# Optimization experiments

Measured on AMD Instinct MI355X. Metric: run time of the kernel, lower is better.

## Reference

```python
import jax, jax.numpy as jnp
import numpy as np
import math

B, T, M, C, H = 2, 2048, 1024, 512, 8
D = C // H  # head dim = 64


def setup_inputs() -> dict:
    key = jax.random.key(0)
    ks = jax.random.split(key, 6)
    return {
        "x": jax.random.normal(ks[0], (B, T, C), jnp.float32),
        "y": jax.random.normal(ks[1], (B, M, C), jnp.float32),
        "attn_x_mask": jnp.ones((1, 1, T, T), jnp.int32),
        "qkv_w": jax.random.normal(ks[2], (3 * C, C), jnp.float32) * 0.02,
        "qkv_b": jax.random.normal(ks[3], (3 * C,), jnp.float32) * 0.02,
        "proj_w": jax.random.normal(ks[4], (C, C), jnp.float32) * 0.02,
        "proj_b": jax.random.normal(ks[5], (C,), jnp.float32) * 0.02,
    }


def _split_heads(t, n, d):
    # [B, N, C] -> [B, H, N, D]
    b = t.shape[0]
    return t.reshape(b, n, H, d).transpose(0, 2, 1, 3)


def reference(x, y, attn_x_mask, qkv_w, qkv_b, proj_w, proj_b):
    b, t, c = x.shape
    m = y.shape[1]
    d = c // H
    scale = 1.0 / math.sqrt(d)

    # shared qkv projection applied to x and y (torch Linear: x @ W.T + b)
    qkv_x = x @ qkv_w.T + qkv_b
    q_x, k_x, v_x = jnp.split(qkv_x, 3, axis=-1)
    qkv_y = y @ qkv_w.T + qkv_b
    q_y, k_y, v_y = jnp.split(qkv_y, 3, axis=-1)

    q_x, k_x, v_x = (_split_heads(a, t, d) for a in (q_x, k_x, v_x))
    q_y, k_y, v_y = (_split_heads(a, m, d) for a in (q_y, k_y, v_y))

    # x -> y cross attention scores (pre-softmax, reused for chaining)
    catt_x2y = jnp.einsum("bhtd,bhmd->bhtm", q_x, k_y) * scale  # [B,H,T,M]
    cval_x2y = jnp.einsum("bhtm,bhmd->bhtd", jax.nn.softmax(catt_x2y, axis=-1), v_y)
    cval_x2y = cval_x2y.transpose(0, 2, 1, 3).reshape(b, t, c)

    # y -> x scores, then chained through raw x2y scores
    catt_y2x = jnp.einsum("bhmd,bhsd->bhms", q_y, k_x) * scale  # [B,H,M,T]
    chained = jnp.einsum("bhtm,bhms->bhts", catt_x2y, catt_y2x) * scale  # [B,H,T,T]
    chained = jnp.where(attn_x_mask == 0, -jnp.inf, chained)
    cval_y2x = jnp.einsum("bhts,bhsd->bhtd", jax.nn.softmax(chained, axis=-1), v_x)
    cval_y2x = cval_y2x.transpose(0, 2, 1, 3).reshape(b, t, c)

    out = cval_x2y - cval_y2x
    out = out @ proj_w.T + proj_b  # dropout layers are identity in eval mode
    return out
```

## Files before the change

### kernel.cpp

```cpp
#include <hip/hip_runtime.h>


typedef _Float16 half_t;
typedef _Float16 half8 __attribute__((ext_vector_type(8)));
typedef _Float16 half4v __attribute__((ext_vector_type(4)));
typedef float floatx4 __attribute__((ext_vector_type(4)));
typedef int int4v __attribute__((ext_vector_type(4)));
typedef int int2v __attribute__((ext_vector_type(2)));

constexpr int Bc = 2, Tc = 2048, Mc = 1024, Cc = 512, Hc = 8, Dc = 64;
constexpr long BTC = (long)Bc * Tc * Cc;
constexpr long ZT  = (long)Bc * Hc * Tc;
constexpr float S1 = 0.18033688f;

enum { EPI_F16STORE = 0, EPI_QKV_XY = 1, EPI_PROJ = 2 };

struct EpiParams {
  half_t* h0;
  half_t* h1;
  half_t* h2;
  half_t* h3;
  half_t* h4;
  half_t* h5;
  half_t* h6;
  float* f0;
  const float* bias;
  float scale;
  int ldc;
  long bstride;
};

__device__ __forceinline__ void gld_lds16(const half_t* g, half_t* l) {
  __builtin_amdgcn_global_load_lds(
      (const __attribute__((address_space(1))) void*)g,
      (__attribute__((address_space(3))) void*)l, 16, 0, 0);
}

__device__ __forceinline__ int pkrtz(float a, float b) {
  return __builtin_bit_cast(int, __builtin_amdgcn_cvt_pkrtz(a, b));
}
__device__ __forceinline__ void pl16(int& a, int& b) {
  asm volatile("v_permlane16_swap_b32 %0, %1" : "+v"(a), "+v"(b));
}
__device__ __forceinline__ void pl32(int& a, int& b) {
  asm volatile("v_permlane32_swap_b32 %0, %1" : "+v"(a), "+v"(b));
}

template <int BM, int BN, int WMG, int WNG, int EPI, int GX = 0, int GY = 0>
__global__ __launch_bounds__(256) void gemm_nt(
    const half_t* __restrict__ A, const half_t* __restrict__ Bt,
    int K, int lda, int ldb, long bsA, long bsB, EpiParams ep)
{
  constexpr int BK = 64;
  constexpr int WTM = BM / WMG, WTN = BN / WNG;
  constexpr int MI = WTM / 16, NI = WTN / 16;
  constexpr int AIT = BM * BK / 8 / 256;
  constexpr int BIT = BN * BK / 8 / 256;
  constexpr int NLD = AIT + BIT;
  __shared__ __align__(16) half_t As[2][BM * BK];
  __shared__ __align__(16) half_t Bs[2][BN * BK];

  const int tid = threadIdx.x;
  const int lane = tid & 63;
  const int wave = tid >> 6;
  const int wm = wave / WNG, wn = wave % WNG;
  const int r16 = lane & 15, g = lane >> 4;
  const int z = blockIdx.z;

  int bxl = blockIdx.x, byl = blockIdx.y;
  if constexpr (GX > 0) {
    constexpr int CHUNK = GX * GY / 8;
    const int f = byl * GX + bxl;
    const int L = (f & 7) * CHUNK + (f >> 3);
    bxl = L % GX; byl = L / GX;
  }
  const long m0 = (long)byl * BM;
  const long n0 = (long)bxl * BN;
  const half_t* Abase = A + (long)z * bsA + m0 * (long)lda;
  const half_t* Bbase = Bt + (long)z * bsB + n0 * (long)ldb;

  const int rA = wm * WTM + r16;
  const int rB = wn * WTN + r16;

  floatx4 acc[MI][NI];
#pragma unroll
  for (int mi = 0; mi < MI; ++mi)
#pragma unroll
    for (int ni = 0; ni < NI; ++ni)
      acc[mi][ni] = floatx4{0.f, 0.f, 0.f, 0.f};

  auto stage = [&](int kt, int buf) {
#pragma unroll
    for (int i = 0; i < AIT; ++i) {
      const int c = tid + i * 256;
      const int row = c >> 3, js = c & 7;
      const int jg = js ^ (row & 7);
      gld_lds16(Abase + (long)row * lda + kt + jg * 8, &As[buf][c * 8]);
    }
#pragma unroll
    for (int i = 0; i < BIT; ++i) {
      const int c = tid + i * 256;
      const int row = c >> 3, js = c & 7;
      const int jg = js ^ (row & 7);
      gld_lds16(Bbase + (long)row * ldb + kt + jg * 8, &Bs[buf][c * 8]);
    }
  };

  const int NIT = K / BK;
  stage(0, 0);
  asm volatile("" ::: "memory");

  for (int it = 0; it < NIT; ++it) {
    const bool hn = (it + 1 < NIT);
    if (hn) stage((it + 1) * BK, (it + 1) & 1);
    asm volatile("" ::: "memory");
    if (hn) {
      if constexpr (NLD == 6) asm volatile("s_waitcnt vmcnt(6)" ::: "memory");
      else if constexpr (NLD == 4) asm volatile("s_waitcnt vmcnt(4)" ::: "memory");
      else if constexpr (NLD == 3) asm volatile("s_waitcnt vmcnt(3)" ::: "memory");
      else if constexpr (NLD == 8) asm volatile("s_waitcnt vmcnt(8)" ::: "memory");
      else asm volatile("s_waitcnt vmcnt(0)" ::: "memory");
    } else {
      asm volatile("s_waitcnt vmcnt(0)" ::: "memory");
    }
    __builtin_amdgcn_s_barrier();
    asm volatile("" ::: "memory");

    const half_t* Ab = As[it & 1];
    const half_t* Bb = Bs[it & 1];
    half8 aF[MI][2], bF[NI][2];
#pragma unroll
    for (int mi = 0; mi < MI; ++mi)
#pragma unroll
      for (int k2 = 0; k2 < 2; ++k2)
        aF[mi][k2] = *reinterpret_cast<const half8*>(
            &Ab[(rA + mi * 16) * BK + ((k2 * 4 + g) ^ (r16 & 7)) * 8]);
#pragma unroll
    for (int ni = 0; ni < NI; ++ni)
#pragma unroll
      for (int k2 = 0; k2 < 2; ++k2)
        bF[ni][k2] = *reinterpret_cast<const half8*>(
            &Bb[(rB + ni * 16) * BK + ((k2 * 4 + g) ^ (r16 & 7)) * 8]);
    __builtin_amdgcn_s_setprio(1);
#pragma unroll
    for (int k2 = 0; k2 < 2; ++k2)
#pragma unroll
      for (int mi = 0; mi < MI; ++mi)
#pragma unroll
        for (int ni = 0; ni < NI; ++ni)
          acc[mi][ni] = __builtin_amdgcn_mfma_f32_16x16x32_f16(
              aF[mi][k2], bF[ni][k2], acc[mi][ni], 0, 0, 0);
    __builtin_amdgcn_s_setprio(0);
    asm volatile("s_waitcnt lgkmcnt(0)" ::: "memory");
    __builtin_amdgcn_s_barrier();
    asm volatile("" ::: "memory");
  }

  half_t* Txp = &As[0][0];
  const bool isx  = (m0 < (long)Bc * Tc);
  const int which = (int)(n0 >> 9);
  const int hh    = ((int)n0 & 511) >> 6;

#pragma unroll
  for (int mi = 0; mi < MI; ++mi) {
#pragma unroll
    for (int ni = 0; ni < NI; ++ni) {
#pragma unroll
      for (int reg = 0; reg < 4; ++reg) {
        const int r = (int)m0 + wm * WTM + mi * 16 + g * 4 + reg;
        const int c = (int)n0 + wn * WTN + ni * 16 + r16;
        const float v = acc[mi][ni][reg];
        if constexpr (EPI == EPI_F16STORE) {
          ep.h0[(long)z * ep.bstride + (long)r * ep.ldc + c] = (half_t)(v * ep.scale);
        } else if constexpr (EPI == EPI_QKV_XY) {
          const float val = v + ep.bias[c];
          const int d = c & 63;
          const int rloc = r - (int)m0;
          if (isx) {
            const int b = (int)(m0 >> 11);
            const int t = r & (Tc - 1);
            const long bh = (long)(b * Hc + hh);
            if (which == 0)      ep.h0[(bh * Tc + t) * Dc + d] = (half_t)(val * S1);
            else if (which == 1) ep.h1[(bh * Tc + t) * Dc + d] = (half_t)val;
            else                 Txp[d * 136 + rloc] = (half_t)val;
          } else {
            const long m2 = m0 - (long)Bc * Tc;
            const int b = (int)(m2 >> 10);
            const int t = (r - Bc * Tc) & (Mc - 1);
            const long bh = (long)(b * Hc + hh);
            if (which == 0)      Txp[d * 136 + rloc] = (half_t)(val * 0.125f);
            else if (which == 1) { ep.h4[(bh * Mc + t) * Dc + d] = (half_t)val;
                                   Txp[d * 136 + rloc] = (half_t)val; }
            else                 Txp[d * 136 + rloc] = (half_t)val;
          }
        } else {
          ep.f0[(long)r * Cc + c] = v + ep.bias[c];
        }
      }
    }
  }

  if constexpr (EPI == EPI_QKV_XY && BM == 128) {
    const bool hasT = isx ? (which == 2) : true;
    if (hasT) {
      __syncthreads();
      half_t* dstT; int L; long tb; int b;
      if (isx) { dstT = ep.h2; L = Tc; tb = m0 & (Tc - 1); b = (int)(m0 >> 11); }
      else {
        const long m2 = m0 - (long)Bc * Tc;
        b = (int)(m2 >> 10); tb = m2 & (Mc - 1); L = Mc;
        dstT = (which == 0) ? ep.h3 : (which == 1) ? ep.h5 : ep.h6;
      }
      const long bh = (long)(b * Hc + hh);
      const int dr = tid >> 2, qd = tid & 3;
      half_t* gbase = dstT + (bh * 64 + dr) * L + tb + qd * 32;
#pragma unroll
      for (int j = 0; j < 4; ++j) {
        const half8 v8 = *reinterpret_cast<const half8*>(&Txp[dr * 136 + qd * 32 + j * 8]);
        *reinterpret_cast<half8*>(&gbase[j * 8]) = v8;
      }
    }
  }
}

__global__ __launch_bounds__(256) void wtq2(
    const half_t* __restrict__ QYT, const half_t* __restrict__ KYT,
    const half_t* __restrict__ QX, half_t* __restrict__ Q2)
{
  __shared__ __align__(16) half_t As[2][4096];
  __shared__ __align__(16) half_t Bs[2][4096];
  __shared__ __align__(16) half_t WTs[4096];
  const int tid = threadIdx.x, lane = tid & 63, wave = tid >> 6;
  const int wm = wave >> 1, wn = wave & 1;
  const int r16 = lane & 15, g = lane >> 4;
  const int f = blockIdx.x;
  const int L = (f & 7) * 64 + (f >> 3);
  const int z = L >> 5;
  const int t0 = (L & 31) * 64;
  const half_t* Aq = QYT + (long)z * Dc * Mc;
  const half_t* Bk = KYT + (long)z * Dc * Mc;

  auto stage1 = [&](int kt, int buf) {
#pragma unroll
    for (int i = 0; i < 2; ++i) {
      const int c = tid + i * 256;
      const int row = c >> 3, js = c & 7, jg = js ^ (row & 7);
      gld_lds16(Aq + (long)row * Mc + kt + jg * 8, &As[buf][c * 8]);
    }
#pragma unroll
    for (int i = 0; i < 2; ++i) {
      const int c = tid + i * 256;
      const int row = c >> 3, js = c & 7, jg = js ^ (row & 7);
      gld_lds16(Bk + (long)row * Mc + kt + jg * 8, &Bs[buf][c * 8]);
    }
  };

  floatx4 acc[2][2];
#pragma unroll
  for (int mi = 0; mi < 2; ++mi)
#pragma unroll
    for (int ni = 0; ni < 2; ++ni) acc[mi][ni] = floatx4{0.f, 0.f, 0.f, 0.f};

  const int rA = wm * 32 + r16, rB = wn * 32 + r16;
  stage1(0, 0);
  asm volatile("" ::: "memory");
  for (int it = 0; it < 16; ++it) {
    const bool hn = (it < 15);
    if (hn) stage1((it + 1) * 64, (it + 1) & 1);
    asm volatile("" ::: "memory");
    if (hn) asm volatile("s_waitcnt vmcnt(4)" ::: "memory");
    else    asm volatile("s_waitcnt vmcnt(0)" ::: "memory");
    __builtin_amdgcn_s_barrier();
    asm volatile("" ::: "memory");
    const half_t* Ab = As[it & 1];
    const half_t* Bb = Bs[it & 1];
    half8 aF[2][2], bF[2][2];
#pragma unroll
    for (int mi = 0; mi < 2; ++mi)
#pragma unroll
      for (int k2 = 0; k2 < 2; ++k2)
        aF[mi][k2] = *reinterpret_cast<const half8*>(
            &Ab[(rA + mi * 16) * 64 + ((k2 * 4 + g) ^ (r16 & 7)) * 8]);
#pragma unroll
    for (int ni = 0; ni < 2; ++ni)
#pragma unroll
      for (int k2 = 0; k2 < 2; ++k2)
        bF[ni][k2] = *reinterpret_cast<const half8*>(
            &Bb[(rB + ni * 16) * 64 + ((k2 * 4 + g) ^ (r16 & 7)) * 8]);
    __builtin_amdgcn_s_setprio(1);
#pragma unroll
    for (int k2 = 0; k2 < 2; ++k2)
#pragma unroll
      for (int mi = 0; mi < 2; ++mi)
#pragma unroll
        for (int ni = 0; ni < 2; ++ni)
          acc[mi][ni] = __builtin_amdgcn_mfma_f32_16x16x32_f16(
              aF[mi][k2], bF[ni][k2], acc[mi][ni], 0, 0, 0);
    __builtin_amdgcn_s_setprio(0);
    asm volatile("s_waitcnt lgkmcnt(0)" ::: "memory");
    __builtin_amdgcn_s_barrier();
    asm volatile("" ::: "memory");
  }

  half_t* P2 = &As[0][0];
#pragma unroll
  for (int i = 0; i < 2; ++i) {
    const int c = tid + i * 256;
    const int row = c >> 3, js = c & 7, jg = js ^ (row & 7);
    gld_lds16(QX + ((long)z * Tc + t0 + row) * 64 + jg * 8, P2 + c * 8);
  }
#pragma unroll
  for (int mi = 0; mi < 2; ++mi)
#pragma unroll
    for (int ni = 0; ni < 2; ++ni)
#pragma unroll
      for (int reg = 0; reg < 4; ++reg) {
        const int r = wm * 32 + mi * 16 + g * 4 + reg;
        const int c = wn * 32 + ni * 16 + r16;
        WTs[r * 64 + (((c >> 3) ^ (r & 7)) << 3) + (c & 7)] =
            (half_t)(acc[mi][ni][reg] * 0.125f);
      }
  __syncthreads();

  floatx4 a2[4];
#pragma unroll
  for (int ni = 0; ni < 4; ++ni) a2[ni] = floatx4{0.f, 0.f, 0.f, 0.f};
  const int rA2 = wave * 16 + r16;
  half8 aF2[2], bF2[4][2];
#pragma unroll
  for (int k2 = 0; k2 < 2; ++k2)
    aF2[k2] = *reinterpret_cast<const half8*>(
        &P2[rA2 * 64 + ((k2 * 4 + g) ^ (r16 & 7)) * 8]);
#pragma unroll
  for (int ni = 0; ni < 4; ++ni)
#pragma unroll
    for (int k2 = 0; k2 < 2; ++k2)
      bF2[ni][k2] = *reinterpret_cast<const half8*>(
          &WTs[(ni * 16 + r16) * 64 + ((k2 * 4 + g) ^ (r16 & 7)) * 8]);
#pragma unroll
  for (int k2 = 0; k2 < 2; ++k2)
#pragma unroll
    for (int ni = 0; ni < 4; ++ni)
      a2[ni] = __builtin_amdgcn_mfma_f32_16x16x32_f16(
          aF2[k2], bF2[ni][k2], a2[ni], 0, 0, 0);
#pragma unroll
  for (int ni = 0; ni < 4; ++ni)
#pragma unroll
    for (int reg = 0; reg < 4; ++reg) {
      const int t = t0 + wave * 16 + g * 4 + reg;
      const int c = ni * 16 + r16;
      Q2[((long)z * Tc + t) * 64 + c] = (half_t)a2[ni][reg];
    }
}

__device__ __forceinline__ void stageK64(const half_t* Kz, int s0, half_t* dst, int tid) {
#pragma unroll
  for (int i = 0; i < 2; ++i) {
    const int c = tid + i * 256;
    const int row = c >> 3, js = c & 7;
    const int jg = js ^ (row & 7);
    gld_lds16(Kz + (long)(s0 + row) * 64 + jg * 8, dst + c * 8);
  }
}
__device__ __forceinline__ void stageV64(const half_t* Vz, int s0, int Slen, half_t* dst, int tid) {
#pragma unroll
  for (int i = 0; i < 2; ++i) {
    const int c = tid + i * 256;
    const int row = c >> 3, js = c & 7;
    const int jg = js ^ (row & 7);
    gld_lds16(Vz + (long)row * Slen + s0 + jg * 8, dst + c * 8);
  }
}

template <bool MASKED>
__device__ __forceinline__ void flash_body(
    const half_t* __restrict__ Qp, const half_t* __restrict__ Kp,
    const half_t* __restrict__ Vp, const unsigned char* __restrict__ mpk,
    half_t* __restrict__ POh, float* __restrict__ Lp,
    int Slen, int sbeg, int z, int q0, half_t* lds)
{
  const int tid = threadIdx.x, lane = tid & 63, w = tid >> 6;
  const int r16 = lane & 15, g = lane >> 4;
  const int b = z >> 3, h = z & 7;
  const int NT = Slen >> 7;
  const half_t* Qz = Qp + ((long)z * Tc + q0) * 64;
  const half_t* Kz = Kp + (long)z * Slen * 64;
  const half_t* Vz = Vp + (long)z * 64 * Slen;
  half_t* Kb0 = lds;
  half_t* Kb1 = lds + 4096;
  half_t* Vb  = lds + 8192;

  stageK64(Kz, sbeg, Kb0, tid);
  asm volatile("" ::: "memory");
  stageV64(Vz, sbeg, Slen, Vb, tid);
  asm volatile("" ::: "memory");

  half8 aQ[2][2];
#pragma unroll
  for (int mi = 0; mi < 2; ++mi)
#pragma unroll
    for (int k2 = 0; k2 < 2; ++k2)
      aQ[mi][k2] = *reinterpret_cast<const half8*>(
          Qz + (w * 32 + mi * 16 + r16) * 64 + k2 * 32 + g * 8);

  half8 vones;
#pragma unroll
  for (int j = 0; j < 8; ++j) vones[j] = (half_t)1.f;

  floatx4 oaccT[2][4];
  floatx4 lacc4[2];
#pragma unroll
  for (int mi = 0; mi < 2; ++mi) {
    lacc4[mi] = floatx4{0.f, 0.f, 0.f, 0.f};
#pragma unroll
    for (int no = 0; no < 4; ++no) oaccT[mi][no] = floatx4{0.f, 0.f, 0.f, 0.f};
  }

  const int send = sbeg + 512;
  int cur = 0;
  for (int s0 = sbeg; s0 < send; s0 += 64) {
    const bool hn = (s0 + 64 < send);
    asm volatile("s_waitcnt vmcnt(2)" ::: "memory");
    __builtin_amdgcn_s_barrier();
    asm volatile("" ::: "memory");

    unsigned int mb32[2];
    if constexpr (MASKED) {
      const int tile = s0 >> 7;
#pragma unroll
      for (int mi = 0; mi < 2; ++mi) {
        const int q = q0 + w * 32 + mi * 16 + r16;
        mb32[mi] = *reinterpret_cast<const unsigned int*>(
            mpk + ((long)q * NT + tile) * 16 + 4 * g);
      }
    }
    const int hf4 = ((s0 >> 6) & 1) ? 4 : 0;
    const unsigned int fullm = hf4 ? 0xf0f0f0f0u : 0x0f0f0f0fu;

    floatx4 sacc[2][4];
#pragma unroll
    for (int mi = 0; mi < 2; ++mi)
#pragma unroll
      for (int ni = 0; ni < 4; ++ni) sacc[mi][ni] = floatx4{0.f, 0.f, 0.f, 0.f};
    const half_t* Kc = cur ? Kb1 : Kb0;
    __builtin_amdgcn_s_setprio(1);
#pragma unroll
    for (int ni = 0; ni < 4; ++ni) {
      const int rB = ni * 16 + r16;
      const half8 b0 = *reinterpret_cast<const half8*>(&Kc[rB * 64 + (g ^ (rB & 7)) * 8]);
      const half8 b1 = *reinterpret_cast<const half8*>(&Kc[rB * 64 + ((4 + g) ^ (rB & 7)) * 8]);
#pragma unroll
      for (int mi = 0; mi < 2; ++mi) {
        sacc[mi][ni] = __builtin_amdgcn_mfma_f32_16x16x32_f16(b0, aQ[mi][0], sacc[mi][ni], 0, 0, 0);
        sacc[mi][ni] = __builtin_amdgcn_mfma_f32_16x16x32_f16(b1, aQ[mi][1], sacc[mi][ni], 0, 0, 0);
      }
    }
    __builtin_amdgcn_s_setprio(0);
    if (hn) stageK64(Kz, s0 + 64, cur ? Kb0 : Kb1, tid);
    asm volatile("" ::: "memory");

#pragma unroll
    for (int mi = 0; mi < 2; ++mi) {
      if constexpr (MASKED) {
        if ((mb32[mi] & fullm) != fullm) {
#pragma unroll
          for (int reg = 0; reg < 4; ++reg)
#pragma unroll
            for (int ni = 0; ni < 4; ++ni)
              if (!((mb32[mi] >> (reg * 8 + ni + hf4)) & 1)) sacc[mi][ni][reg] = -__builtin_inff();
        }
      }
#pragma unroll
      for (int ni = 0; ni < 4; ++ni)
#pragma unroll
        for (int reg = 0; reg < 4; ++reg)
          sacc[mi][ni][reg] = __builtin_amdgcn_exp2f(sacc[mi][ni][reg]);
    }

    if (hn) { asm volatile("s_waitcnt vmcnt(2)" ::: "memory"); }
    else    { asm volatile("s_waitcnt vmcnt(0)" ::: "memory"); }
    __builtin_amdgcn_s_barrier();
    asm volatile("" ::: "memory");

#pragma unroll
    for (int c = 0; c < 2; ++c) {
      half8 bVv[4];
#pragma unroll
      for (int no = 0; no < 4; ++no) {
        const int rV = no * 16 + r16;
        bVv[no] = *reinterpret_cast<const half8*>(
            &Vb[rV * 64 + ((c * 4 + g) ^ (rV & 7)) * 8]);
      }
#pragma unroll
      for (int mi = 0; mi < 2; ++mi) {
        int x0 = pkrtz(sacc[mi][2 * c][0],     sacc[mi][2 * c][1]);
        int x1 = pkrtz(sacc[mi][2 * c][2],     sacc[mi][2 * c][3]);
        int x2 = pkrtz(sacc[mi][2 * c + 1][0], sacc[mi][2 * c + 1][1]);
        int x3 = pkrtz(sacc[mi][2 * c + 1][2], sacc[mi][2 * c + 1][3]);
        pl32(x0, x2); pl32(x1, x3);
        pl16(x0, x2); pl16(x1, x3);
        int4v wv; wv[0] = x0; wv[1] = x1; wv[2] = x2; wv[3] = x3;
        const half8 aP = __builtin_bit_cast(half8, wv);
        __builtin_amdgcn_s_setprio(1);
#pragma unroll
        for (int no = 0; no < 4; ++no)
          oaccT[mi][no] = __builtin_amdgcn_mfma_f32_16x16x32_f16(bVv[no], aP, oaccT[mi][no], 0, 0, 0);
        lacc4[mi] = __builtin_amdgcn_mfma_f32_16x16x32_f16(vones, aP, lacc4[mi], 0, 0, 0);
        __builtin_amdgcn_s_setprio(0);
      }
    }
    __builtin_amdgcn_s_barrier();
    asm volatile("" ::: "memory");
    if (hn) stageV64(Vz, s0 + 64, Slen, Vb, tid);
    asm volatile("" ::: "memory");
    cur ^= 1;
  }

  float ls2[2];
#pragma unroll
  for (int mi = 0; mi < 2; ++mi) ls2[mi] = lacc4[mi][0];

  float* slab = reinterpret_cast<float*>(lds) + w * 1024;
#pragma unroll
  for (int mi = 0; mi < 2; ++mi) {
    const int tq = q0 + w * 32 + mi * 16;
    if (lane < 16) Lp[(long)z * Tc + tq + r16] = ls2[mi];
#pragma unroll
    for (int no = 0; no < 4; ++no) {
      floatx4 v = oaccT[mi][no];
      *reinterpret_cast<floatx4*>(&slab[r16 * 64 + no * 16 + (g ^ (r16 & 3)) * 4]) = v;
    }
#pragma unroll
    for (int it = 0; it < 4; ++it) {
      const int q2 = it * 4 + g;
      const int d4 = r16;
      const floatx4 v = *reinterpret_cast<const floatx4*>(
          &slab[q2 * 64 + (d4 >> 2) * 16 + ((d4 & 3) ^ (q2 & 3)) * 4]);
      const long off = ((long)(b * Tc + tq + q2)) * Cc + h * 64 + d4 * 4;
      half4v hh; hh[0] = (half_t)v[0]; hh[1] = (half_t)v[1];
      hh[2] = (half_t)v[2]; hh[3] = (half_t)v[3];
      __builtin_nontemporal_store(__builtin_bit_cast(int2v, hh),
                                  reinterpret_cast<int2v*>(&POh[off]));
    }
  }
}

__global__ __launch_bounds__(256, 4) void flash_both(
    const half_t* __restrict__ Q2, const half_t* __restrict__ KX,
    const half_t* __restrict__ VXT, const unsigned char* __restrict__ mpk,
    const half_t* __restrict__ QX, const half_t* __restrict__ KY,
    const half_t* __restrict__ VYT,
    half_t* __restrict__ POh, float* __restrict__ Lp)
{
  __shared__ __align__(16) half_t lds[12288];
  const int bx = blockIdx.x;
  if (bx < 1024) {
    const int z  = ((bx & 7) << 1) | ((bx >> 3) & 1);
    const int qt = (bx >> 4) & 3;
    const int q0 = (bx >> 6) * 128;
    flash_body<true>(Q2, KX, VXT, mpk,
                     POh + (long)qt * BTC, Lp + (long)qt * ZT,
                     Tc, qt * 512, z, q0, lds);
  } else {
    const int b2 = bx - 1024;
    const int z  = ((b2 & 7) << 1) | ((b2 >> 3) & 1);
    const int sh = (b2 >> 4) & 1;
    const int q0 = (b2 >> 5) * 128;
    flash_body<false>(QX, KY, VYT, nullptr,
                      POh + (long)(4 + sh) * BTC, Lp + (long)(4 + sh) * ZT,
                      Mc, sh * 512, z, q0, lds);
  }
}

__global__ __launch_bounds__(256) void combine_k(
    const half_t* __restrict__ POh, const float* __restrict__ Lp,
    half_t* __restrict__ DH)
{
  const long idx = (long)blockIdx.x * 256 + threadIdx.x;
  const long c8 = idx * 8;
  const int c = (int)(c8 & (Cc - 1));
  const long bt = c8 >> 9;
  const int h = c >> 6;
  const int b = (int)(bt >> 11), t = (int)(bt & (Tc - 1));
  const long zt = (long)(b * Hc + h) * Tc + t;
  const float i0 = 1.f / (Lp[zt] + Lp[ZT + zt] + Lp[2 * ZT + zt] + Lp[3 * ZT + zt]);
  const float i1 = 1.f / (Lp[4 * ZT + zt] + Lp[5 * ZT + zt]);
  half8 o[6];
#pragma unroll
  for (int s = 0; s < 6; ++s)
    o[s] = __builtin_bit_cast(half8, __builtin_nontemporal_load(
        reinterpret_cast<const int4v*>(POh) + s * (BTC / 8) + idx));
  half8 r;
#pragma unroll
  for (int j = 0; j < 8; ++j) {
    float a0 = 0.f, a1 = 0.f;
#pragma unroll
    for (int s = 0; s < 4; ++s) a0 += (float)o[s][j];
#pragma unroll
    for (int s = 4; s < 6; ++s) a1 += (float)o[s][j];
    r[j] = (half_t)(a1 * i1 - a0 * i0);
  }
  *reinterpret_cast<half8*>(&DH[c8]) = r;
}

__device__ __forceinline__ void cvt4(const float* in, half_t* out, long i) {
  const float4 f = reinterpret_cast<const float4*>(in)[i];
  half4v h; h[0] = (half_t)f.x; h[1] = (half_t)f.y; h[2] = (half_t)f.z; h[3] = (half_t)f.w;
  reinterpret_cast<half4v*>(out)[i] = h;
}

__global__ __launch_bounds__(256) void prep(
    const float* __restrict__ x, const float* __restrict__ y,
    const float* __restrict__ qw, const float* __restrict__ pw,
    const int* __restrict__ mask,
    half_t* __restrict__ XH, half_t* __restrict__ YH,
    half_t* __restrict__ WQ, half_t* __restrict__ WP,
    unsigned char* __restrict__ mpk)
{
  const long i = (long)blockIdx.x * 256 + threadIdx.x;
  constexpr long n0 = 524288;
  constexpr long n1 = n0 + 262144;
  constexpr long n2 = n1 + 196608;
  constexpr long n3 = n2 + 65536;
  if (i < n0) cvt4(x, XH, i);
  else if (i < n1) cvt4(y, YH, i - n0);
  else if (i < n2) cvt4(qw, WQ, i - n1);
  else if (i < n3) cvt4(pw, WP, i - n2);
  else {
    const long idx = i - n3;
    const int t = (int)(idx >> 8), tile = (int)((idx >> 4) & 15), r16 = (int)(idx & 15);
    const int* row = mask + (long)t * Tc + tile * 128 + r16;
    unsigned int bbits = 0;
#pragma unroll
    for (int ni = 0; ni < 8; ++ni)
      bbits |= (row[ni * 16] != 0 ? 1u : 0u) << ni;
    mpk[idx] = (unsigned char)bbits;
  }
}

constexpr size_t OFF_XH   = 0;
constexpr size_t OFF_YH   = OFF_XH   + (size_t)Bc*Tc*Cc*2;
constexpr size_t OFF_WQ   = OFF_YH   + (size_t)Bc*Mc*Cc*2;
constexpr size_t OFF_WP   = OFF_WQ   + (size_t)3*Cc*Cc*2;
constexpr size_t OFF_QX   = OFF_WP   + (size_t)Cc*Cc*2;
constexpr size_t OFF_KX   = OFF_QX   + (size_t)Bc*Hc*Tc*Dc*2;
constexpr size_t OFF_VXT  = OFF_KX   + (size_t)Bc*Hc*Tc*Dc*2;
constexpr size_t OFF_QYT  = OFF_VXT  + (size_t)Bc*Hc*Tc*Dc*2;
constexpr size_t OFF_KY   = OFF_QYT  + (size_t)Bc*Hc*Mc*Dc*2;
constexpr size_t OFF_KYT  = OFF_KY   + (size_t)Bc*Hc*Mc*Dc*2;
constexpr size_t OFF_VYT  = OFF_KYT  + (size_t)Bc*Hc*Mc*Dc*2;
constexpr size_t OFF_Q2   = OFF_VYT  + (size_t)Bc*Hc*Mc*Dc*2;
constexpr size_t OFF_DH   = OFF_Q2   + (size_t)Bc*Hc*Tc*Dc*2;
constexpr size_t OFF_MPK  = OFF_DH   + (size_t)Bc*Tc*Cc*2;
constexpr size_t OFF_PO   = OFF_MPK  + (size_t)Tc*256;
constexpr size_t OFF_L    = OFF_PO   + (size_t)6*BTC*2;

extern "C" void kernel_launch(void* const* d_in, const int* in_sizes, int n_in,
                              void* d_out, int out_size, void* d_ws, size_t ws_size,
                              hipStream_t stream) {
  const float* x      = (const float*)d_in[0];
  const float* y      = (const float*)d_in[1];
  const int*   mask   = (const int*)  d_in[2];
  const float* qkv_b  = (const float*)d_in[4];
  const float* proj_b = (const float*)d_in[6];
  float* out = (float*)d_out;
  char* ws = (char*)d_ws;

  half_t* XH   = (half_t*)(ws + OFF_XH);
  half_t* YH   = (half_t*)(ws + OFF_YH);
  half_t* WQ   = (half_t*)(ws + OFF_WQ);
  half_t* WP   = (half_t*)(ws + OFF_WP);
  half_t* QX   = (half_t*)(ws + OFF_QX);
  half_t* KX   = (half_t*)(ws + OFF_KX);
  half_t* VXT  = (half_t*)(ws + OFF_VXT);
  half_t* QYT  = (half_t*)(ws + OFF_QYT);
  half_t* KY   = (half_t*)(ws + OFF_KY);
  half_t* KYT  = (half_t*)(ws + OFF_KYT);
  half_t* VYT  = (half_t*)(ws + OFF_VYT);
  half_t* Q2   = (half_t*)(ws + OFF_Q2);
  half_t* DH   = (half_t*)(ws + OFF_DH);
  unsigned char* MPK = (unsigned char*)(ws + OFF_MPK);
  half_t* POh  = (half_t*)(ws + OFF_PO);
  float*  Lp   = (float*) (ws + OFF_L);

  prep<<<6144, 256, 0, stream>>>(x, y, (const float*)d_in[3], (const float*)d_in[5],
                                 mask, XH, YH, WQ, WP, MPK);

  {
    EpiParams ep{};
    ep.h0 = QX; ep.h1 = KX; ep.h2 = VXT; ep.h3 = QYT;
    ep.h4 = KY; ep.h5 = KYT; ep.h6 = VYT; ep.bias = qkv_b;
    gemm_nt<128,64,2,2,EPI_QKV_XY,24,48><<<dim3(24, 48, 1), 256, 0, stream>>>(
        XH, WQ, Cc, Cc, Cc, 0, 0, ep);
  }

  wtq2<<<dim3(512), 256, 0, stream>>>(QYT, KYT, QX, Q2);

  flash_both<<<dim3(1536), 256, 0, stream>>>(
      Q2, KX, VXT, MPK, QX, KY, VYT, POh, Lp);

  combine_k<<<(int)(BTC/8/256), 256, 0, stream>>>(POh, Lp, DH);

  {
    EpiParams ep{}; ep.f0 = out; ep.bias = proj_b;
    gemm_nt<64,32,2,2,EPI_PROJ,16,64><<<dim3(16, 64, 1), 256, 0, stream>>>(
        DH, WP, Cc, Cc, Cc, 0, 0, ep);
  }
}
```

Before: 168.8 us.

## Co-schedule wtq2 with x2y attention and launch chained attention separately

Moves the independent x-to-y flash attention blocks out of the combined flash kernel and launches them in one grid alongside the wtq2 blocks that build Q2. The chained attention, which needs Q2, then runs in its own launch. This is meant to fill the GPU while the small wtq2 kernel runs, removing its idle tail and a serial dependency. In exchange the merged kernel must reserve the larger wtq2 LDS footprint (20480 halves), which may lower occupancy for the x2y flash blocks.

New measurement: 169.2 us. Within noise of the previous version (+0.2%).

```diff
diff --git a/kernel.cpp b/kernel.cpp
--- a/kernel.cpp
+++ b/kernel.cpp
@@ -223,35 +223,35 @@
   }
 }
 
-__global__ __launch_bounds__(256) void wtq2(
+__device__ __forceinline__ void wtq2_body(
     const half_t* __restrict__ QYT, const half_t* __restrict__ KYT,
-    const half_t* __restrict__ QX, half_t* __restrict__ Q2)
+    const half_t* __restrict__ QX, half_t* __restrict__ Q2,
+    int f, half_t* lds)
 {
-  __shared__ __align__(16) half_t As[2][4096];
-  __shared__ __align__(16) half_t Bs[2][4096];
-  __shared__ __align__(16) half_t WTs[4096];
   const int tid = threadIdx.x, lane = tid & 63, wave = tid >> 6;
   const int wm = wave >> 1, wn = wave & 1;
   const int r16 = lane & 15, g = lane >> 4;
-  const int f = blockIdx.x;
   const int L = (f & 7) * 64 + (f >> 3);
   const int z = L >> 5;
   const int t0 = (L & 31) * 64;
   const half_t* Aq = QYT + (long)z * Dc * Mc;
   const half_t* Bk = KYT + (long)z * Dc * Mc;
+  half_t* WTs = lds + 16384;
 
   auto stage1 = [&](int kt, int buf) {
+    half_t* Asb = lds + buf * 4096;
+    half_t* Bsb = lds + 8192 + buf * 4096;
 #pragma unroll
     for (int i = 0; i < 2; ++i) {
       const int c = tid + i * 256;
       const int row = c >> 3, js = c & 7, jg = js ^ (row & 7);
-      gld_lds16(Aq + (long)row * Mc + kt + jg * 8, &As[buf][c * 8]);
+      gld_lds16(Aq + (long)row * Mc + kt + jg * 8, &Asb[c * 8]);
     }
 #pragma unroll
     for (int i = 0; i < 2; ++i) {
       const int c = tid + i * 256;
       const int row = c >> 3, js = c & 7, jg = js ^ (row & 7);
-      gld_lds16(Bk + (long)row * Mc + kt + jg * 8, &Bs[buf][c * 8]);
+      gld_lds16(Bk + (long)row * Mc + kt + jg * 8, &Bsb[c * 8]);
     }
   };
 
@@ -272,8 +272,8 @@
     else    asm volatile("s_waitcnt vmcnt(0)" ::: "memory");
     __builtin_amdgcn_s_barrier();
     asm volatile("" ::: "memory");
-    const half_t* Ab = As[it & 1];
-    const half_t* Bb = Bs[it & 1];
+    const half_t* Ab = lds + (it & 1) * 4096;
+    const half_t* Bb = lds + 8192 + (it & 1) * 4096;
     half8 aF[2][2], bF[2][2];
 #pragma unroll
     for (int mi = 0; mi < 2; ++mi)
@@ -302,7 +302,7 @@
     asm volatile("" ::: "memory");
   }
 
-  half_t* P2 = &As[0][0];
+  half_t* P2 = lds;
 #pragma unroll
   for (int i = 0; i < 2; ++i) {
     const int c = tid + i * 256;
@@ -545,31 +545,39 @@
   }
 }
 
-__global__ __launch_bounds__(256, 4) void flash_both(
+__global__ __launch_bounds__(256, 4) void wtq2_att1(
+    const half_t* __restrict__ QYT, const half_t* __restrict__ KYT,
+    const half_t* __restrict__ QX, half_t* __restrict__ Q2,
+    const half_t* __restrict__ KY, const half_t* __restrict__ VYT,
+    half_t* __restrict__ POh, float* __restrict__ Lp)
+{
+  __shared__ __align__(16) half_t lds[20480];
+  const int bx = blockIdx.x;
+  if (bx < 512) {
+    const int z  = ((bx & 7) << 1) | ((bx >> 3) & 1);
+    const int sh = (bx >> 4) & 1;
+    const int q0 = (bx >> 5) * 128;
+    flash_body<false>(QX, KY, VYT, nullptr,
+                      POh + (long)(4 + sh) * BTC, Lp + (long)(4 + sh) * ZT,
+                      Mc, sh * 512, z, q0, lds);
+  } else {
+    wtq2_body(QYT, KYT, QX, Q2, bx - 512, lds);
+  }
+}
+
+__global__ __launch_bounds__(256, 4) void flash_att0(
     const half_t* __restrict__ Q2, const half_t* __restrict__ KX,
     const half_t* __restrict__ VXT, const unsigned char* __restrict__ mpk,
-    const half_t* __restrict__ QX, const half_t* __restrict__ KY,
-    const half_t* __restrict__ VYT,
     half_t* __restrict__ POh, float* __restrict__ Lp)
 {
   __shared__ __align__(16) half_t lds[12288];
   const int bx = blockIdx.x;
-  if (bx < 1024) {
-    const int z  = ((bx & 7) << 1) | ((bx >> 3) & 1);
-    const int qt = (bx >> 4) & 3;
-    const int q0 = (bx >> 6) * 128;
-    flash_body<true>(Q2, KX, VXT, mpk,
-                     POh + (long)qt * BTC, Lp + (long)qt * ZT,
-                     Tc, qt * 512, z, q0, lds);
-  } else {
-    const int b2 = bx - 1024;
-    const int z  = ((b2 & 7) << 1) | ((b2 >> 3) & 1);
-    const int sh = (b2 >> 4) & 1;
-    const int q0 = (b2 >> 5) * 128;
-    flash_body<false>(QX, KY, VYT, nullptr,
-                      POh + (long)(4 + sh) * BTC, Lp + (long)(4 + sh) * ZT,
-                      Mc, sh * 512, z, q0, lds);
-  }
+  const int z  = ((bx & 7) << 1) | ((bx >> 3) & 1);
+  const int qt = (bx >> 4) & 3;
+  const int q0 = (bx >> 6) * 128;
+  flash_body<true>(Q2, KX, VXT, mpk,
+                   POh + (long)qt * BTC, Lp + (long)qt * ZT,
+                   Tc, qt * 512, z, q0, lds);
 }
 
 __global__ __launch_bounds__(256) void combine_k(
@@ -694,10 +702,9 @@
         XH, WQ, Cc, Cc, Cc, 0, 0, ep);
   }
 
-  wtq2<<<dim3(512), 256, 0, stream>>>(QYT, KYT, QX, Q2);
-
-  flash_both<<<dim3(1536), 256, 0, stream>>>(
-      Q2, KX, VXT, MPK, QX, KY, VYT, POh, Lp);
+  wtq2_att1<<<dim3(1024), 256, 0, stream>>>(QYT, KYT, QX, Q2, KY, VYT, POh, Lp);
+
+  flash_att0<<<dim3(1024), 256, 0, stream>>>(Q2, KX, VXT, MPK, POh, Lp);
 
   combine_k<<<(int)(BTC/8/256), 256, 0, stream>>>(POh, Lp, DH);
 
```
